# Kernel optimization log

Measured on AMD Instinct MI355X. Metric: run time of the kernel, lower is better.

Reference implementation:

```python
import jax, jax.numpy as jnp
from jax import lax
import numpy as np

B, T, C, V, E, H, OC = 1024, 32, 14, 21128, 200, 50, 8


def gru(x, Wih, Whh, bih, bhh):
    # x: [N, T, E] -> hiddens [N, T, H]; torch nn.GRU gate order (r, z, n)
    Hd = Whh.shape[1]
    xp = jnp.einsum('nte,ge->ntg', x, Wih) + bih  # [N, T, 3H]
    h0 = jnp.zeros((x.shape[0], Hd), x.dtype)

    def step(h, xt):
        gh = h @ Whh.T + bhh
        r = jax.nn.sigmoid(xt[:, :Hd] + gh[:, :Hd])
        z = jax.nn.sigmoid(xt[:, Hd:2 * Hd] + gh[:, Hd:2 * Hd])
        n = jnp.tanh(xt[:, 2 * Hd:] + r * gh[:, 2 * Hd:])
        h_new = (1.0 - z) * n + z * h
        return h_new, h_new

    _, hs = lax.scan(step, h0, jnp.swapaxes(xp, 0, 1))
    return jnp.swapaxes(hs, 0, 1)


def setup_inputs():
    key = jax.random.key(0)
    ks = jax.random.split(key, 32)
    s = 0.1
    inp = {
        'contexts_indices': jax.random.randint(ks[0], (B, T), 0, V),
        'candidates_indices': jax.random.randint(ks[1], (B, C, T), 0, V),
        'y_dev': jax.random.uniform(ks[2], (B, C), dtype=jnp.float32),
        'emb': jax.random.normal(ks[3], (V, E), dtype=jnp.float32),
        'A': jax.random.normal(ks[4], (H, H), dtype=jnp.float32) * s,
        'Wih_c': jax.random.normal(ks[5], (3 * H, E), dtype=jnp.float32) * s,
        'Whh_c': jax.random.normal(ks[6], (3 * H, H), dtype=jnp.float32) * s,
        'bih_c': jnp.zeros((3 * H,), jnp.float32),
        'bhh_c': jnp.zeros((3 * H,), jnp.float32),
        'Wih_r': jax.random.normal(ks[7], (3 * H, E), dtype=jnp.float32) * s,
        'Whh_r': jax.random.normal(ks[8], (3 * H, H), dtype=jnp.float32) * s,
        'bih_r': jnp.zeros((3 * H,), jnp.float32),
        'bhh_r': jnp.zeros((3 * H,), jnp.float32),
        'conv_w': jax.random.normal(ks[9], (OC, 2, 3, 3), dtype=jnp.float32) * s,
        'Wih2': jax.random.normal(ks[10], (3 * H, OC * 10 * 10), dtype=jnp.float32) * s,
        'Whh2': jax.random.normal(ks[11], (3 * H, H), dtype=jnp.float32) * s,
        'bih2': jnp.zeros((3 * H,), jnp.float32),
        'bhh2': jnp.zeros((3 * H,), jnp.float32),
        'fc1_w': jax.random.normal(ks[12], (100, C * H), dtype=jnp.float32) * s,
        'fc1_b': jnp.zeros((100,), jnp.float32),
        'fc2_w': jax.random.normal(ks[13], (C, 100), dtype=jnp.float32) * s,
        'fc2_b': jnp.zeros((C,), jnp.float32),
    }
    return inp


def reference(contexts_indices, candidates_indices, y_dev, emb, A,
              Wih_c, Whh_c, bih_c, bhh_c, Wih_r, Whh_r, bih_r, bhh_r,
              conv_w, Wih2, Whh2, bih2, bhh2, fc1_w, fc1_b, fc2_w, fc2_b):
    b = contexts_indices.shape[0]
    ctx = contexts_indices[:, None, :]                      # [B,1,T]
    ctx_emb = emb[ctx]                                      # [B,1,T,E] (dropout = identity in eval)
    cand_emb = emb[candidates_indices]                      # [B,C,T,E]

    ctx_h = gru(ctx_emb.reshape(-1, T, E), Wih_c, Whh_c, bih_c, bhh_c).reshape(b, 1, T, H)
    cand_h = gru(cand_emb.reshape(-1, T, E), Wih_r, Whh_r, bih_r, bhh_r).reshape(b, C, T, H)

    M1 = jnp.einsum('btph,bcqh->btcpq', ctx_emb, cand_emb)  # [B,1,C,T,T]
    ctx_hA = jnp.einsum('btij,jk->btik', ctx_h, A)
    M2 = jnp.einsum('btph,bcqh->btcpq', ctx_hA, cand_h)

    # faithful to torch: stack on dim 2 then row-major view(-1, 2, T, T)
    M = jnp.stack([M1, M2], axis=2).reshape(-1, 2, T, T)    # [B*C, 2, T, T]

    conv = lax.conv_general_dilated(M, conv_w, (1, 1), 'VALID',
                                    dimension_numbers=('NCHW', 'OIHW', 'NCHW'))  # [B*C, OC, 30, 30]
    pooled = lax.reduce_window(conv, -jnp.inf, lax.max,
                               (1, 1, 3, 3), (1, 1, 3, 3), 'VALID')              # [B*C, OC, 10, 10]

    feats = pooled.reshape(b, C, OC * 10 * 10)              # [B, C, 800]
    Hs = gru(feats, Wih2, Whh2, bih2, bhh2)                 # [B, C, H]
    flat = Hs.reshape(b, -1)                                # [B, C*H]

    hid = jax.nn.relu(flat @ fc1_w.T + fc1_b)
    log_probs = jax.nn.log_softmax(hid @ fc2_w.T + fc2_b, axis=-1)  # softmax then log
    kl = jnp.where(y_dev > 0, y_dev * (jnp.log(y_dev) - log_probs), 0.0)
    return jnp.mean(kl)
```

## Files before the change

### kernel.cpp

```cpp
#include <hip/hip_runtime.h>
#include <math.h>

typedef unsigned short u16;
typedef short s16;
typedef u16 u16x8 __attribute__((ext_vector_type(8)));
typedef s16 short8v __attribute__((ext_vector_type(8)));
typedef float f32x4 __attribute__((ext_vector_type(4)));

__device__ __forceinline__ float b2f(u16 u) {
    return __uint_as_float(((unsigned)u) << 16);
}
__device__ __forceinline__ u16 f2b(float f) {
    unsigned u = __float_as_uint(f);
    unsigned r = (u + 0x7FFFu + ((u >> 16) & 1u)) >> 16;
    return (u16)r;
}

__global__ __launch_bounds__(256) void k_cvt4(
    const float* __restrict__ s0, u16* __restrict__ d0, long n0,
    const float* __restrict__ s1, u16* __restrict__ d1, long n1,
    const float* __restrict__ s2, u16* __restrict__ d2, long n2,
    const float* __restrict__ s3, u16* __restrict__ d3, long n3)
{
    long j = (long)blockIdx.x * 256 + threadIdx.x;
    const float* s; u16* d;
    if (j < n0) { s = s0; d = d0; }
    else {
        j -= n0;
        if (j < n1) { s = s1; d = d1; }
        else {
            j -= n1;
            if (j < n2) { s = s2; d = d2; }
            else {
                j -= n2;
                if (j < n3) { s = s3; d = d3; }
                else return;
            }
        }
    }
    float4 v = ((const float4*)s)[j];
    *(ushort4*)(d + j * 4) = make_ushort4(f2b(v.x), f2b(v.y), f2b(v.z), f2b(v.w));
}

__global__ __launch_bounds__(256) void k_projmm2(
    const u16* __restrict__ embh, const u16* __restrict__ wc,
    const u16* __restrict__ wr, const float* __restrict__ bc,
    const float* __restrict__ br, float* __restrict__ outc,
    u16* __restrict__ outr, int V)
{
    __shared__ s16 Ab[2048];
    __shared__ s16 Bb[2560];
    __shared__ float bhL[160];
    const int t = threadIdx.x;
    const int w = t >> 6, l = t & 63, lg = l >> 4, lr = l & 15;
    int id = blockIdx.x;
    const int half = (id >= 662) ? 1 : 0;
    id -= half * 662;
    const u16* wh = half ? wr : wc;
    const float* bias = half ? br : bc;
    const int mb = id >> 1, nb = id & 1;
    const long rowbase = (long)mb * 64;
    const int colbase = nb * 80;
    if (t < 160) bhL[t] = (t < 150) ? bias[t] : 0.f;

    f32x4 acc[5];
#pragma unroll
    for (int i = 0; i < 5; ++i) acc[i] = (f32x4){0,0,0,0};

    for (int ch = 0; ch < 7; ++ch) {
        __syncthreads();
        {
            int kc = t >> 6, row = t & 63;
            long grow = rowbase + row; if (grow >= V) grow = V - 1;
            int k0 = ch * 32 + kc * 8;
            short8v v = {0,0,0,0,0,0,0,0};
            if (k0 < 200) v = *(const short8v*)(embh + grow * 200 + k0);
            *(short8v*)&Ab[t * 8] = v;
        }
        for (int it = t; it < 320; it += 256) {
            int kc = it / 80, col = it % 80;
            int gcol = colbase + col;
            int k0 = ch * 32 + kc * 8;
            short8v v = {0,0,0,0,0,0,0,0};
            if (gcol < 150 && k0 < 200)
                v = *(const short8v*)(wh + (size_t)gcol * 200 + k0);
            *(short8v*)&Bb[it * 8] = v;
        }
        __syncthreads();
        short8v a = *(short8v*)&Ab[(lg * 64 + w * 16 + lr) * 8];
#pragma unroll
        for (int ct = 0; ct < 5; ++ct) {
            short8v bv = *(short8v*)&Bb[(lg * 80 + ct * 16 + lr) * 8];
            acc[ct] = __builtin_amdgcn_mfma_f32_16x16x32_bf16(a, bv, acc[ct], 0, 0, 0);
        }
    }
#pragma unroll
    for (int ct = 0; ct < 5; ++ct) {
        int gcol = colbase + ct * 16 + lr;
        if (gcol < 150) {
#pragma unroll
            for (int rr = 0; rr < 4; ++rr) {
                long row = rowbase + w * 16 + lg * 4 + rr;
                float vv = acc[ct][rr] + bhL[gcol];
                if (half) outr[row * 152 + gcol] = f2b(vv);
                else      outc[row * 152 + gcol] = vv;
            }
        }
    }
}

template<int MODE, int SEQS>
__global__ __launch_bounds__(256) void k_gru_scan(
    const void* __restrict__ xp_, const int* __restrict__ idx,
    const float* __restrict__ Whh, const float* __restrict__ bhh,
    void* __restrict__ hs_, int T)
{
    __shared__ s16  hbuf[1024];
    __shared__ float ghL[SEQS * 160];
    __shared__ float hL[SEQS * 52];
    __shared__ float bhL[152];
    __shared__ u16 xraw[4864];
    const int t = threadIdx.x;
    const int w = t >> 6, l = t & 63, lg = l >> 4, lr = l & 15;
    constexpr int HST = (MODE == 2) ? 56 : 50;
    constexpr int XROW = SEQS * 152;
    u16*   xbH = xraw;
    float* xbF = (float*)xraw;

    for (int li = t; li < 1024; li += 256) hbuf[li] = 0;
    for (int e = t; e < SEQS * 52; e += 256) hL[e] = 0.f;
    if (t < 152) bhL[t] = (t < 150) ? bhh[t] : 0.f;

    const int te_0 = (w * 3     > 9) ? 9 : w * 3;
    const int te_1 = (w * 3 + 1 > 9) ? 9 : w * 3 + 1;
    const int te_2 = (w * 3 + 2 > 9) ? 9 : w * 3 + 2;
    short8v B00 = {0,0,0,0,0,0,0,0}, B01 = B00, B10 = B00, B11 = B00, B20 = B00, B21 = B00;
    {
        int cols[3] = { te_0 * 16 + lr, te_1 * 16 + lr, te_2 * 16 + lr };
        short8v* frg[6] = { &B00, &B01, &B10, &B11, &B20, &B21 };
#pragma unroll
        for (int ti = 0; ti < 3; ++ti) {
            int col = cols[ti];
            if (col < 150) {
#pragma unroll
                for (int s = 0; s < 2; ++s) {
                    short8v v = {0,0,0,0,0,0,0,0};
#pragma unroll
                    for (int e = 0; e < 8; ++e) {
                        int k = (s * 4 + lg) * 8 + e;
                        if (k < 50) v[e] = (s16)f2b(Whh[col * 50 + k]);
                    }
                    *frg[ti * 2 + s] = v;
                }
            }
        }
    }

    const long seqbase = (long)blockIdx.x * SEQS;
    const float* xpf = (const float*)xp_;
    const u16*   xph = (const u16*)xp_;
    float* hsf = (float*)hs_;
    u16*   hsh = (u16*)hs_;

    const int rA = (MODE == 2) ? t / 19 : t / 38;
    const int oA = (MODE == 2) ? (t % 19) * 8 : (t % 38) * 4;
    const int rB = (MODE == 2) ? (t + 256) / 19 : (t + 256) / 38;
    const int oB = (MODE == 2) ? ((t + 256) % 19) * 8 : ((t + 256) % 38) * 4;
    const bool actA = (MODE == 2) ? (t < SEQS * 19) : true;
    const bool hasB = (MODE == 2) ? (t + 256 < SEQS * 19) : (t + 256 < SEQS * 38);

    auto rowbase = [&](int rr, int stp) -> size_t {
        long r = seqbase + rr;
        long src = (MODE == 0) ? (r * T + stp) : (long)idx[r * T + stp];
        return (size_t)src * 152;
    };

    if (MODE == 2) {
        if (actA) *(u16x8*)&xbH[rA * 152 + oA] = *(const u16x8*)(xph + rowbase(rA, 0) + oA);
        if (hasB) *(u16x8*)&xbH[rB * 152 + oB] = *(const u16x8*)(xph + rowbase(rB, 0) + oB);
    } else {
        *(float4*)&xbF[rA * 152 + oA] = *(const float4*)(xpf + rowbase(rA, 0) + oA);
        if (hasB)
            *(float4*)&xbF[rB * 152 + oB] = *(const float4*)(xpf + rowbase(rB, 0) + oB);
    }
    __syncthreads();

    for (int st = 0; st < T; ++st) {
        const int cur = st & 1;
        u16x8 pfh0, pfh1;
        float4 pf0, pf1;
        if (st + 1 < T) {
            if (MODE == 2) {
                if (actA) pfh0 = *(const u16x8*)(xph + rowbase(rA, st + 1) + oA);
                if (hasB) pfh1 = *(const u16x8*)(xph + rowbase(rB, st + 1) + oB);
            } else {
                pf0 = *(const float4*)(xpf + rowbase(rA, st + 1) + oA);
                if (hasB) pf1 = *(const float4*)(xpf + rowbase(rB, st + 1) + oB);
            }
        }
        short8v a0 = *(short8v*)&hbuf[((0 + lg) * 16 + lr) * 8];
        short8v a1 = *(short8v*)&hbuf[((4 + lg) * 16 + lr) * 8];
        f32x4 c0 = {0,0,0,0}, c1 = {0,0,0,0}, c2 = {0,0,0,0};
        c0 = __builtin_amdgcn_mfma_f32_16x16x32_bf16(a0, B00, c0, 0, 0, 0);
        c0 = __builtin_amdgcn_mfma_f32_16x16x32_bf16(a1, B01, c0, 0, 0, 0);
        c1 = __builtin_amdgcn_mfma_f32_16x16x32_bf16(a0, B10, c1, 0, 0, 0);
        c1 = __builtin_amdgcn_mfma_f32_16x16x32_bf16(a1, B11, c1, 0, 0, 0);
        c2 = __builtin_amdgcn_mfma_f32_16x16x32_bf16(a0, B20, c2, 0, 0, 0);
        c2 = __builtin_amdgcn_mfma_f32_16x16x32_bf16(a1, B21, c2, 0, 0, 0);
        if (lg * 4 < SEQS) {
            int col0 = te_0 * 16 + lr, col1 = te_1 * 16 + lr, col2 = te_2 * 16 + lr;
            if (col0 < 150) {
#pragma unroll
                for (int r = 0; r < 4; ++r) ghL[(lg * 4 + r) * 160 + col0] = c0[r] + bhL[col0];
            }
            if (col1 < 150) {
#pragma unroll
                for (int r = 0; r < 4; ++r) ghL[(lg * 4 + r) * 160 + col1] = c1[r] + bhL[col1];
            }
            if (col2 < 150) {
#pragma unroll
                for (int r = 0; r < 4; ++r) ghL[(lg * 4 + r) * 160 + col2] = c2[r] + bhL[col2];
            }
        }
        __syncthreads();
        if (st + 1 < T) {
            if (MODE == 2) {
                if (actA) *(u16x8*)&xbH[(cur ^ 1) * XROW + rA * 152 + oA] = pfh0;
                if (hasB) *(u16x8*)&xbH[(cur ^ 1) * XROW + rB * 152 + oB] = pfh1;
            } else {
                *(float4*)&xbF[(cur ^ 1) * XROW + rA * 152 + oA] = pf0;
                if (hasB) *(float4*)&xbF[(cur ^ 1) * XROW + rB * 152 + oB] = pf1;
            }
        }
        for (int item = t; item < SEQS * 50; item += 256) {
            int ss = item / 50, hh = item % 50;
            float xv0, xv1, xv2;
            if (MODE == 2) {
                const u16* xr = &xbH[cur * XROW + ss * 152];
                xv0 = b2f(xr[hh]); xv1 = b2f(xr[50 + hh]); xv2 = b2f(xr[100 + hh]);
            } else {
                const float* xr = &xbF[cur * XROW + ss * 152];
                xv0 = xr[hh]; xv1 = xr[50 + hh]; xv2 = xr[100 + hh];
            }
            float vr  = xv0 + ghL[ss * 160 + hh];
            float vz  = xv1 + ghL[ss * 160 + 50 + hh];
            float ghn = ghL[ss * 160 + 100 + hh];
            float rg = 1.f / (1.f + __expf(-vr));
            float zg = 1.f / (1.f + __expf(-vz));
            float a = xv2 + rg * ghn;
            a = fminf(fmaxf(a, -15.f), 15.f);
            float e2 = __expf(-2.f * a);
            float nn2 = (1.f - e2) / (1.f + e2);
            float hn = (1.f - zg) * nn2 + zg * hL[ss * 52 + hh];
            hL[ss * 52 + hh] = hn;
            hbuf[((hh >> 3) * 16 + ss) * 8 + (hh & 7)] = (s16)f2b(hn);
            size_t ofs = ((size_t)(seqbase + ss) * T + st) * HST + hh;
            if (MODE == 2) hsh[ofs] = f2b(hn); else hsf[ofs] = hn;
        }
        __syncthreads();
    }
}

__global__ __launch_bounds__(256) void k_matA(
    const float* __restrict__ inp, const float* __restrict__ A,
    float* __restrict__ outp)
{
    __shared__ float AL[50 * 52];
    __shared__ float inL[32 * 52];
    const int t = threadIdx.x;
    for (int e = t; e < 2500; e += 256) AL[(e / 50) * 52 + (e % 50)] = A[e];
    const long rbase = (long)blockIdx.x * 32;
    for (int e = t; e < 1600; e += 256) {
        int r = e / 50, j = e % 50;
        inL[r * 52 + j] = inp[(rbase + r) * 50 + j];
    }
    __syncthreads();
    for (int item = t; item < 1600; item += 256) {
        int r = item / 50, kk = item % 50;
        float acc = 0.f;
#pragma unroll 10
        for (int j = 0; j < 50; ++j)
            acc += inL[r * 52 + j] * AL[j * 52 + kk];
        outp[(rbase + r) * 50 + kk] = acc;
    }
}

__global__ __launch_bounds__(256) void k_matchconv(
    const u16* __restrict__ embh, const int* __restrict__ ctx_idx,
    const int* __restrict__ cand_idx, const float* __restrict__ ctxA,
    const u16* __restrict__ candh_h, const float* __restrict__ conv_w,
    u16* __restrict__ feats, int b0)
{
    __shared__ s16 pool16[9480];
    __shared__ float wL[144];
    __shared__ int ci[32], qi[2][32];
    u16* Mb    = (u16*)pool16;
    u16* convL = (u16*)pool16 + 2184;
    const int t = threadIdx.x;
    const int wg = blockIdx.x;
    const int xcd = wg & 7, q = wg >> 3;
    const int r = q % 14, bq = q / 14;
    const int b = b0 + bq * 8 + xcd;
    const long nl = (long)(bq * 8 + xcd) * 14 + r;
    const int w = t >> 6, l = t & 63, lg = l >> 4, lr = l & 15;

    if (t < 144) wL[t] = conv_w[t];

    f32x4 cacc0 = {0,0,0,0}, cacc1 = {0,0,0,0};
    const int job0 = w * 2, job1 = w * 2 + 1;
    const int ch0 = job0 >> 2, rt0 = (job0 >> 1) & 1, ct0 = job0 & 1;
    const int ch1 = job1 >> 2, rt1 = (job1 >> 1) & 1, ct1 = job1 & 1;

    if (r < 7) {
        const int c0 = 2 * r;
        if (t < 32) ci[t] = ctx_idx[b * 32 + t];
        else if (t < 96)
            qi[(t - 32) >> 5][t & 31] =
                cand_idx[((long)b * 14 + c0 + ((t - 32) >> 5)) * 32 + (t & 31)];
        __syncthreads();
        s16* ctxL = pool16;
        s16* canL = pool16 + 3168;
#pragma unroll
        for (int cnk = 0; cnk < 3; ++cnk) {
            const int kcbase = (cnk == 0) ? 0 : (cnk == 1 ? 12 : 20);
            const int kccnt  = (cnk == 0) ? 12 : 8;
            const int scnt   = (cnk == 0) ? 3 : 2;
            if (cnk) __syncthreads();
            for (int it = t; it < kccnt * 32; it += 256) {
                int kcl = it >> 5, row = it & 31;
                int kc = kcbase + kcl;
                short8v v = {0,0,0,0,0,0,0,0};
                if (kc < 25) v = *(const short8v*)(embh + (size_t)ci[row] * 200 + kc * 8);
                *(short8v*)&ctxL[(kcl * 33 + row) * 8] = v;
            }
            for (int it = t; it < kccnt * 64; it += 256) {
                int kcl = it >> 6, col = it & 63;
                int kc = kcbase + kcl;
                short8v v = {0,0,0,0,0,0,0,0};
                if (kc < 25)
                    v = *(const short8v*)(embh + (size_t)qi[col >> 5][col & 31] * 200 + kc * 8);
                *(short8v*)&canL[(kcl * 65 + col) * 8] = v;
            }
            __syncthreads();
            for (int sl = 0; sl < scnt; ++sl) {
                int kcl = sl * 4 + lg;
                short8v a0 = *(short8v*)&ctxL[(kcl * 33 + rt0 * 16 + lr) * 8];
                short8v b0 = *(short8v*)&canL[(kcl * 65 + ch0 * 32 + ct0 * 16 + lr) * 8];
                short8v b1 = *(short8v*)&canL[(kcl * 65 + ch1 * 32 + ct1 * 16 + lr) * 8];
                cacc0 = __builtin_amdgcn_mfma_f32_16x16x32_bf16(a0, b0, cacc0, 0, 0, 0);
                short8v a1 = (rt0 == rt1) ? a0
                           : *(short8v*)&ctxL[(kcl * 33 + rt1 * 16 + lr) * 8];
                cacc1 = __builtin_amdgcn_mfma_f32_16x16x32_bf16(a1, b1, cacc1, 0, 0, 0);
            }
        }
    } else {
        const int c0 = 2 * (r - 7);
        s16* aL = pool16;
        s16* cL = pool16 + 2112;
        for (int it = t; it < 256; it += 256) {
            int kc = it >> 5, row = it & 31;
            const float* src = ctxA + ((long)b * 32 + row) * 50;
            short8v v = {0,0,0,0,0,0,0,0};
#pragma unroll
            for (int e = 0; e < 8; ++e) {
                int k = kc * 8 + e;
                if (k < 50) v[e] = (s16)f2b(src[k]);
            }
            *(short8v*)&aL[(kc * 33 + row) * 8] = v;
        }
        for (int it = t; it < 512; it += 256) {
            int kc = it >> 6, col = it & 63;
            long row = ((long)(b - b0) * 14 + c0 + (col >> 5)) * 32 + (col & 31);
            short8v v = {0,0,0,0,0,0,0,0};
            if (kc < 7) {
                v = *(const short8v*)(candh_h + (size_t)row * 56 + kc * 8);
                if (kc == 6) { v[2] = 0; v[3] = 0; v[4] = 0; v[5] = 0; v[6] = 0; v[7] = 0; }
            }
            *(short8v*)&cL[(kc * 65 + col) * 8] = v;
        }
        __syncthreads();
#pragma unroll
        for (int sl = 0; sl < 2; ++sl) {
            int kcl = sl * 4 + lg;
            short8v a0 = *(short8v*)&aL[(kcl * 33 + rt0 * 16 + lr) * 8];
            short8v b0 = *(short8v*)&cL[(kcl * 65 + ch0 * 32 + ct0 * 16 + lr) * 8];
            short8v b1 = *(short8v*)&cL[(kcl * 65 + ch1 * 32 + ct1 * 16 + lr) * 8];
            cacc0 = __builtin_amdgcn_mfma_f32_16x16x32_bf16(a0, b0, cacc0, 0, 0, 0);
            short8v a1 = (rt0 == rt1) ? a0
                       : *(short8v*)&aL[(kcl * 33 + rt1 * 16 + lr) * 8];
            cacc1 = __builtin_amdgcn_mfma_f32_16x16x32_bf16(a1, b1, cacc1, 0, 0, 0);
        }
    }

    __syncthreads();
#pragma unroll
    for (int rr = 0; rr < 4; ++rr) {
        Mb[ch0 * 1092 + (rt0 * 16 + lg * 4 + rr) * 33 + ct0 * 16 + lr] = f2b(cacc0[rr]);
        Mb[ch1 * 1092 + (rt1 * 16 + lg * 4 + rr) * 33 + ct1 * 16 + lr] = f2b(cacc1[rr]);
    }

    short8v Bc = {0,0,0,0,0,0,0,0};
    int dlt[8];
#pragma unroll
    for (int e = 0; e < 8; ++e) {
        int s = lg * 8 + e;
        if (s < 18) {
            int ch = s / 9, r9 = s % 9, ky = r9 / 3, kx = r9 % 3;
            dlt[e] = ch * 1092 + ky * 33 + kx;
            if (lr < 8) Bc[e] = (s16)f2b(wL[lr * 18 + s]);
        } else dlt[e] = 0;
    }
    __syncthreads();

    for (int tile = w; tile < 57; tile += 4) {
        int m = tile * 16 + lr;
        int cy = m / 30, cx = m - cy * 30;
        int base = cy * 33 + cx;
        short8v a;
#pragma unroll
        for (int e = 0; e < 8; ++e) a[e] = (s16)Mb[base + dlt[e]];
        f32x4 c = {0,0,0,0};
        c = __builtin_amdgcn_mfma_f32_16x16x32_bf16(a, Bc, c, 0, 0, 0);
        if (lr < 8) {
#pragma unroll
            for (int rr = 0; rr < 4; ++rr)
                convL[(tile * 16 + lg * 4 + rr) * 8 + lr] = f2b(c[rr]);
        }
    }
    __syncthreads();

    for (int item = t; item < 800; item += 256) {
        int oc = item / 100, rem = item % 100, py = rem / 10, px = rem % 10;
        int m0 = (3 * py) * 30 + 3 * px;
        float mx = -1e30f;
#pragma unroll
        for (int dy = 0; dy < 3; ++dy)
#pragma unroll
            for (int dx = 0; dx < 3; ++dx)
                mx = fmaxf(mx, b2f(convL[(m0 + dy * 30 + dx) * 8 + oc]));
        feats[nl * 800 + item] = f2b(mx);
    }
}

__global__ __launch_bounds__(256) void k_xp2mm(
    const u16* __restrict__ feats, const u16* __restrict__ w2h,
    const float* __restrict__ bih2, float* __restrict__ out)
{
    __shared__ s16 Ab[2048];
    __shared__ s16 Bb[2560];
    __shared__ float bhL[160];
    const int t = threadIdx.x;
    const int w = t >> 6, l = t & 63, lg = l >> 4, lr = l & 15;
    const int mb = blockIdx.x >> 1, nb = blockIdx.x & 1;
    const long rowbase = (long)mb * 64;
    const int colbase = nb * 80;
    if (t < 160) bhL[t] = (t < 150) ? bih2[t] : 0.f;

    f32x4 acc[5];
#pragma unroll
    for (int i = 0; i < 5; ++i) acc[i] = (f32x4){0,0,0,0};

    for (int ch = 0; ch < 25; ++ch) {
        __syncthreads();
        {
            int kc = t >> 6, row = t & 63;
            *(short8v*)&Ab[t * 8] =
                *(const short8v*)(feats + (rowbase + row) * 800 + ch * 32 + kc * 8);
        }
        for (int it = t; it < 320; it += 256) {
            int kc = it / 80, col = it % 80;
            int gcol = colbase + col;
            short8v v = {0,0,0,0,0,0,0,0};
            if (gcol < 150)
                v = *(const short8v*)(w2h + (size_t)gcol * 800 + ch * 32 + kc * 8);
            *(short8v*)&Bb[it * 8] = v;
        }
        __syncthreads();
        short8v a = *(short8v*)&Ab[(lg * 64 + w * 16 + lr) * 8];
#pragma unroll
        for (int ct = 0; ct < 5; ++ct) {
            short8v bv = *(short8v*)&Bb[(lg * 80 + ct * 16 + lr) * 8];
            acc[ct] = __builtin_amdgcn_mfma_f32_16x16x32_bf16(a, bv, acc[ct], 0, 0, 0);
        }
    }
#pragma unroll
    for (int ct = 0; ct < 5; ++ct) {
        int gcol = colbase + ct * 16 + lr;
        if (gcol < 150) {
#pragma unroll
            for (int rr = 0; rr < 4; ++rr) {
                long row = rowbase + w * 16 + lg * 4 + rr;
                out[row * 152 + gcol] = acc[ct][rr] + bhL[gcol];
            }
        }
    }
}

__global__ __launch_bounds__(128) void k_head(
    const float* __restrict__ Hs, const float* __restrict__ w1,
    const float* __restrict__ b1, const float* __restrict__ w2,
    const float* __restrict__ b2, const float* __restrict__ y,
    float* __restrict__ partial)
{
    __shared__ float hr[700];
    __shared__ float hidL[100];
    const int t = threadIdx.x;
    const long b = blockIdx.x;
    for (int e = t; e < 700; e += 128) hr[e] = Hs[b * 700 + e];
    __syncthreads();
    if (t < 100) {
        float acc = b1[t];
        const float4* wp = (const float4*)(w1 + (size_t)t * 700);
        for (int k4 = 0; k4 < 175; ++k4) {
            float4 wv = wp[k4];
            float4 hv = *(float4*)&hr[k4 * 4];
            acc += wv.x * hv.x + wv.y * hv.y + wv.z * hv.z + wv.w * hv.w;
        }
        hidL[t] = fmaxf(acc, 0.f);
    }
    __syncthreads();
    if (t < 64) {
        float logit = -1e30f;
        if (t < 14) {
            logit = b2[t];
            for (int k = 0; k < 100; ++k) logit += hidL[k] * w2[t * 100 + k];
        }
        float m = logit;
        for (int off = 8; off; off >>= 1) m = fmaxf(m, __shfl_xor(m, off, 16));
        float ex = (t < 14) ? __expf(logit - m) : 0.f;
        float se = ex;
        for (int off = 8; off; off >>= 1) se += __shfl_xor(se, off, 16);
        float kl = 0.f;
        if (t < 14) {
            float lp = logit - m - __logf(se);
            float yv = y[b * 14 + t];
            kl = (yv > 0.f) ? yv * (__logf(yv) - lp) : 0.f;
        }
        for (int off = 8; off; off >>= 1) kl += __shfl_xor(kl, off, 16);
        if (t == 0) partial[b] = kl;
    }
}

__global__ __launch_bounds__(256) void k_reduce(
    const float* __restrict__ partial, float* __restrict__ out)
{
    __shared__ float sm[256];
    const int t = threadIdx.x;
    sm[t] = partial[t] + partial[t + 256] + partial[t + 512] + partial[t + 768];
    __syncthreads();
    for (int off = 128; off; off >>= 1) {
        if (t < off) sm[t] += sm[t + off];
        __syncthreads();
    }
    if (t == 0) out[0] = sm[0] * (1.f / 14336.f);
}

extern "C" void kernel_launch(void* const* d_in, const int* in_sizes, int n_in,
                              void* d_out, int out_size, void* d_ws, size_t ws_size,
                              hipStream_t stream)
{
    const int*   ctx_idx  = (const int*)d_in[0];
    const int*   cand_idx = (const int*)d_in[1];
    const float* y_dev    = (const float*)d_in[2];
    const float* emb      = (const float*)d_in[3];
    const float* A        = (const float*)d_in[4];
    const float* Wih_c    = (const float*)d_in[5];
    const float* Whh_c    = (const float*)d_in[6];
    const float* bih_c    = (const float*)d_in[7];
    const float* bhh_c    = (const float*)d_in[8];
    const float* Wih_r    = (const float*)d_in[9];
    const float* Whh_r    = (const float*)d_in[10];
    const float* bih_r    = (const float*)d_in[11];
    const float* bhh_r    = (const float*)d_in[12];
    const float* conv_w   = (const float*)d_in[13];
    const float* Wih2     = (const float*)d_in[14];
    const float* Whh2     = (const float*)d_in[15];
    const float* bih2     = (const float*)d_in[16];
    const float* bhh2     = (const float*)d_in[17];
    const float* fc1_w    = (const float*)d_in[18];
    const float* fc1_b    = (const float*)d_in[19];
    const float* fc2_w    = (const float*)d_in[20];
    const float* fc2_b    = (const float*)d_in[21];

    float* ws = (float*)d_ws;
    u16*   embh    = (u16*)ws;
    float* proj_c  = ws + 2112800;
    u16*   proj_rh = (u16*)(ws + 5332768);
    float* ctx_h   = ws + 6942752;
    float* ctxA    = ws + 8581152;
    u16*   candh_h = (u16*)(ws + 10219552);
    u16*   feats_h = (u16*)(ws + 23064608);
    u16*   w2h     = (u16*)(ws + 28799008);
    u16*   wch     = (u16*)(ws + 28859008);
    u16*   wrh     = (u16*)(ws + 28874008);
    float* xp2     = ws + 28889008;
    float* hs2     = ws + 31068080;
    float* part    = ws + 31784880;

    k_cvt4 <<<4303, 256, 0, stream>>>(emb, embh, 1056400,
                                      Wih2, w2h, 30000,
                                      Wih_c, wch, 7500,
                                      Wih_r, wrh, 7500);
    k_projmm2 <<<1324, 256, 0, stream>>>(embh, wch, wrh, bih_c, bih_r,
                                         proj_c, proj_rh, 21128);
    k_gru_scan<1, 8> <<<128, 256, 0, stream>>>(proj_c, ctx_idx,  Whh_c, bhh_c, ctx_h, 32);
    k_gru_scan<2, 16><<<896, 256, 0, stream>>>(proj_rh, cand_idx, Whh_r, bhh_r, candh_h, 32);
    k_matA <<<1024, 256, 0, stream>>>(ctx_h, A, ctxA);
    k_matchconv <<<14336, 256, 0, stream>>>(embh, ctx_idx, cand_idx, ctxA, candh_h,
                                            conv_w, feats_h, 0);
    k_xp2mm <<<448, 256, 0, stream>>>(feats_h, w2h, bih2, xp2);
    k_gru_scan<0, 8> <<<128, 256, 0, stream>>>(xp2, nullptr, Whh2, bhh2, hs2, 14);
    k_head <<<1024, 128, 0, stream>>>(hs2, fc1_w, fc1_b, fc2_w, fc2_b, y_dev, part);
    k_reduce <<<1, 256, 0, stream>>>(part, (float*)d_out);
}
```

Baseline: 379.4 us.

## Merge context and candidate GRU scans into one launch with bf16 intermediates

The context GRU scan, previously its own 128-block launch with fp32 projections and 8 sequences per block, now runs inside a single 960-block kernel alongside the candidate scan. It uses the bf16 16-sequence mode, which removes one serial kernel and gives the short context scan work to overlap with. The context projection, context hidden states and ctx*A product are now stored as bf16 with stride 56, halving their traffic and letting matchconv load ctxA with vector loads. The cost is lower precision on the context path.

```diff
diff --git a/kernel.cpp b/kernel.cpp
--- a/kernel.cpp
+++ b/kernel.cpp
@@ -45,7 +45,7 @@
 __global__ __launch_bounds__(256) void k_projmm2(
     const u16* __restrict__ embh, const u16* __restrict__ wc,
     const u16* __restrict__ wr, const float* __restrict__ bc,
-    const float* __restrict__ br, float* __restrict__ outc,
+    const float* __restrict__ br, u16* __restrict__ outc,
     u16* __restrict__ outr, int V)
 {
     __shared__ s16 Ab[2048];
@@ -58,6 +58,7 @@
     id -= half * 662;
     const u16* wh = half ? wr : wc;
     const float* bias = half ? br : bc;
+    u16* outp = half ? outr : outc;
     const int mb = id >> 1, nb = id & 1;
     const long rowbase = (long)mb * 64;
     const int colbase = nb * 80;
@@ -101,19 +102,17 @@
 #pragma unroll
             for (int rr = 0; rr < 4; ++rr) {
                 long row = rowbase + w * 16 + lg * 4 + rr;
-                float vv = acc[ct][rr] + bhL[gcol];
-                if (half) outr[row * 152 + gcol] = f2b(vv);
-                else      outc[row * 152 + gcol] = vv;
+                outp[row * 152 + gcol] = f2b(acc[ct][rr] + bhL[gcol]);
             }
         }
     }
 }
 
 template<int MODE, int SEQS>
-__global__ __launch_bounds__(256) void k_gru_scan(
+__device__ __forceinline__ void gru_body(
     const void* __restrict__ xp_, const int* __restrict__ idx,
     const float* __restrict__ Whh, const float* __restrict__ bhh,
-    void* __restrict__ hs_, int T)
+    void* __restrict__ hs_, int T, long blk)
 {
     __shared__ s16  hbuf[1024];
     __shared__ float ghL[SEQS * 160];
@@ -156,7 +155,7 @@
         }
     }
 
-    const long seqbase = (long)blockIdx.x * SEQS;
+    const long seqbase = blk * SEQS;
     const float* xpf = (const float*)xp_;
     const u16*   xph = (const u16*)xp_;
     float* hsf = (float*)hs_;
@@ -261,9 +260,33 @@
     }
 }
 
+__global__ __launch_bounds__(256) void k_scan_all(
+    const u16* __restrict__ proj_ch, const u16* __restrict__ proj_rh,
+    const int* __restrict__ ctx_idx, const int* __restrict__ cand_idx,
+    const float* __restrict__ Whh_c, const float* __restrict__ Whh_r,
+    const float* __restrict__ bhh_c, const float* __restrict__ bhh_r,
+    u16* __restrict__ ctx_hh, u16* __restrict__ candh_h)
+{
+    const long bid = blockIdx.x;
+    const bool cand = (bid < 896);
+    gru_body<2, 16>(cand ? (const void*)proj_rh : (const void*)proj_ch,
+                    cand ? cand_idx : ctx_idx,
+                    cand ? Whh_r : Whh_c,
+                    cand ? bhh_r : bhh_c,
+                    cand ? (void*)candh_h : (void*)ctx_hh,
+                    32, cand ? bid : bid - 896);
+}
+
+__global__ __launch_bounds__(256) void k_scan2(
+    const float* __restrict__ xp2, const float* __restrict__ Whh2,
+    const float* __restrict__ bhh2, float* __restrict__ hs2)
+{
+    gru_body<0, 8>(xp2, nullptr, Whh2, bhh2, hs2, 14, (long)blockIdx.x);
+}
+
 __global__ __launch_bounds__(256) void k_matA(
-    const float* __restrict__ inp, const float* __restrict__ A,
-    float* __restrict__ outp)
+    const u16* __restrict__ inh, const float* __restrict__ A,
+    u16* __restrict__ outh)
 {
     __shared__ float AL[50 * 52];
     __shared__ float inL[32 * 52];
@@ -272,7 +295,7 @@
     const long rbase = (long)blockIdx.x * 32;
     for (int e = t; e < 1600; e += 256) {
         int r = e / 50, j = e % 50;
-        inL[r * 52 + j] = inp[(rbase + r) * 50 + j];
+        inL[r * 52 + j] = b2f(inh[(rbase + r) * 56 + j]);
     }
     __syncthreads();
     for (int item = t; item < 1600; item += 256) {
@@ -281,13 +304,13 @@
 #pragma unroll 10
         for (int j = 0; j < 50; ++j)
             acc += inL[r * 52 + j] * AL[j * 52 + kk];
-        outp[(rbase + r) * 50 + kk] = acc;
+        outh[(rbase + r) * 56 + kk] = f2b(acc);
     }
 }
 
 __global__ __launch_bounds__(256) void k_matchconv(
     const u16* __restrict__ embh, const int* __restrict__ ctx_idx,
-    const int* __restrict__ cand_idx, const float* __restrict__ ctxA,
+    const int* __restrict__ cand_idx, const u16* __restrict__ ctxA_h,
     const u16* __restrict__ candh_h, const float* __restrict__ conv_w,
     u16* __restrict__ feats, int b0)
 {
@@ -359,12 +382,10 @@
         s16* cL = pool16 + 2112;
         for (int it = t; it < 256; it += 256) {
             int kc = it >> 5, row = it & 31;
-            const float* src = ctxA + ((long)b * 32 + row) * 50;
             short8v v = {0,0,0,0,0,0,0,0};
-#pragma unroll
-            for (int e = 0; e < 8; ++e) {
-                int k = kc * 8 + e;
-                if (k < 50) v[e] = (s16)f2b(src[k]);
+            if (kc < 7) {
+                v = *(const short8v*)(ctxA_h + (size_t)(b * 32 + row) * 56 + kc * 8);
+                if (kc == 6) { v[2] = 0; v[3] = 0; v[4] = 0; v[5] = 0; v[6] = 0; v[7] = 0; }
             }
             *(short8v*)&aL[(kc * 33 + row) * 8] = v;
         }
@@ -584,32 +605,33 @@
 
     float* ws = (float*)d_ws;
     u16*   embh    = (u16*)ws;
-    float* proj_c  = ws + 2112800;
-    u16*   proj_rh = (u16*)(ws + 5332768);
-    float* ctx_h   = ws + 6942752;
-    float* ctxA    = ws + 8581152;
-    u16*   candh_h = (u16*)(ws + 10219552);
-    u16*   feats_h = (u16*)(ws + 23064608);
-    u16*   w2h     = (u16*)(ws + 28799008);
-    u16*   wch     = (u16*)(ws + 28859008);
-    u16*   wrh     = (u16*)(ws + 28874008);
-    float* xp2     = ws + 28889008;
-    float* hs2     = ws + 31068080;
-    float* part    = ws + 31784880;
+    u16*   proj_ch = (u16*)(ws + 2112800);
+    u16*   proj_rh = (u16*)(ws + 3722784);
+    u16*   ctx_hh  = (u16*)(ws + 5332768);
+    u16*   ctxA_h  = (u16*)(ws + 6250272);
+    u16*   candh_h = (u16*)(ws + 7167776);
+    u16*   feats_h = (u16*)(ws + 20012832);
+    u16*   w2h     = (u16*)(ws + 25747232);
+    u16*   wch     = (u16*)(ws + 25807232);
+    u16*   wrh     = (u16*)(ws + 25822232);
+    float* xp2     = ws + 25837232;
+    float* hs2     = ws + 28016304;
+    float* part    = ws + 28733104;
 
     k_cvt4 <<<4303, 256, 0, stream>>>(emb, embh, 1056400,
                                       Wih2, w2h, 30000,
                                       Wih_c, wch, 7500,
                                       Wih_r, wrh, 7500);
     k_projmm2 <<<1324, 256, 0, stream>>>(embh, wch, wrh, bih_c, bih_r,
-                                         proj_c, proj_rh, 21128);
-    k_gru_scan<1, 8> <<<128, 256, 0, stream>>>(proj_c, ctx_idx,  Whh_c, bhh_c, ctx_h, 32);
-    k_gru_scan<2, 16><<<896, 256, 0, stream>>>(proj_rh, cand_idx, Whh_r, bhh_r, candh_h, 32);
-    k_matA <<<1024, 256, 0, stream>>>(ctx_h, A, ctxA);
-    k_matchconv <<<14336, 256, 0, stream>>>(embh, ctx_idx, cand_idx, ctxA, candh_h,
+                                         proj_ch, proj_rh, 21128);
+    k_scan_all <<<960, 256, 0, stream>>>(proj_ch, proj_rh, ctx_idx, cand_idx,
+                                         Whh_c, Whh_r, bhh_c, bhh_r,
+                                         ctx_hh, candh_h);
+    k_matA <<<1024, 256, 0, stream>>>(ctx_hh, A, ctxA_h);
+    k_matchconv <<<14336, 256, 0, stream>>>(embh, ctx_idx, cand_idx, ctxA_h, candh_h,
                                             conv_w, feats_h, 0);
     k_xp2mm <<<448, 256, 0, stream>>>(feats_h, w2h, bih2, xp2);
-    k_gru_scan<0, 8> <<<128, 256, 0, stream>>>(xp2, nullptr, Whh2, bhh2, hs2, 14);
+    k_scan2 <<<128, 256, 0, stream>>>(xp2, Whh2, bhh2, hs2);
     k_head <<<1024, 128, 0, stream>>>(hs2, fc1_w, fc1_b, fc2_w, fc2_b, y_dev, part);
     k_reduce <<<1, 256, 0, stream>>>(part, (float*)d_out);
 }
```

Result: faster. 330.6 us (-12.9%).
